# Kernel tuning notes

Measured on AMD Instinct MI355X. Metric: run time of the kernel, lower is better.

## Reference

```python
import jax, jax.numpy as jnp
import numpy as np

NUM_SKILLS = 1000
DIM_S = 64
SIZE_M = 64
B, T = 64, 200


def setup_inputs() -> dict:
    key = jax.random.key(0)
    ks = jax.random.split(key, 16)
    skills = jax.random.randint(ks[0], (B, T), 0, NUM_SKILLS)
    responses = jax.random.randint(ks[1], (B, T), 0, 2)
    s = 1.0 / np.sqrt(DIM_S)
    return {
        "skills": skills,
        "responses": responses,
        "k_emb": jax.random.normal(ks[2], (NUM_SKILLS, DIM_S)) * s,
        "v_emb": jax.random.normal(ks[3], (2 * NUM_SKILLS, DIM_S)) * s,
        "Mk": jax.random.normal(ks[4], (SIZE_M, DIM_S)) * np.sqrt(2.0 / DIM_S),
        "Mv0": jax.random.normal(ks[5], (SIZE_M, DIM_S)) * np.sqrt(2.0 / DIM_S),
        "fW": jax.random.normal(ks[6], (DIM_S, 2 * DIM_S)) * (1.0 / np.sqrt(2 * DIM_S)),
        "fb": jnp.zeros((DIM_S,)),
        "eW": jax.random.normal(ks[7], (DIM_S, DIM_S)) * s,
        "eb": jnp.zeros((DIM_S,)),
        "aW": jax.random.normal(ks[8], (DIM_S, DIM_S)) * s,
        "ab": jnp.zeros((DIM_S,)),
        "pW": jax.random.normal(ks[9], (1, DIM_S)) * s,
        "pb": jnp.zeros((1,)),
    }


def reference(skills, responses, k_emb, v_emb, Mk, Mv0, fW, fb, eW, eb, aW, ab, pW, pb):
    # dropout is identity in eval mode
    masked_r = responses * (responses > -1).astype(responses.dtype)
    x = skills + NUM_SKILLS * masked_r            # [B, T]
    k = k_emb[skills]                              # [B, T, D]
    v = v_emb[x]                                   # [B, T, D]
    w = jax.nn.softmax(jnp.einsum('btd,md->btm', k, Mk), axis=-1)  # [B, T, M]
    e = jax.nn.sigmoid(v @ eW.T + eb)              # [B, T, D]
    a = jnp.tanh(v @ aW.T + ab)                    # [B, T, D]

    Mv_init = jnp.broadcast_to(Mv0, (skills.shape[0],) + Mv0.shape)  # [B, M, D]

    def step(Mvt, inp):
        wt, et, at = inp                           # [B,M], [B,D], [B,D]
        read = jnp.einsum('bm,bmd->bd', wt, Mvt)   # read BEFORE update (Mv[:, :-1])
        Mvt = Mvt * (1.0 - wt[:, :, None] * et[:, None, :]) + wt[:, :, None] * at[:, None, :]
        return Mvt, read

    xs = (jnp.swapaxes(w, 0, 1), jnp.swapaxes(e, 0, 1), jnp.swapaxes(a, 0, 1))
    _, reads = jax.lax.scan(step, Mv_init, xs)     # reads: [T, B, D]
    reads = jnp.swapaxes(reads, 0, 1)              # [B, T, D]

    f = jnp.tanh(jnp.concatenate([reads, k], axis=-1) @ fW.T + fb)  # [B, T, D]
    p = jax.nn.sigmoid(f @ pW.T + pb)[..., 0]      # [B, T]
    return p[:, 1:]                                # pred, [B, T-1]
```

## Files before the change

kernel.cpp:

```cpp
#include <hip/hip_runtime.h>
#include <hip/hip_bf16.h>
#include <stdint.h>

#define NSK 1000
#define TT  200
#define BB  64
#define NROW (BB * TT)
#define NOUT (BB * (TT-1))
#define CH  20
#define RW  8

__device__ __forceinline__ float lane_bcast(float v, int l) {
  return __uint_as_float(__builtin_amdgcn_readlane(__float_as_uint(v), l));
}
__device__ __forceinline__ unsigned ulane_bcast(unsigned v, int l) {
  return __builtin_amdgcn_readlane(v, l);
}
__device__ __forceinline__ float frcp(float x) { return __builtin_amdgcn_rcpf(x); }
__device__ __forceinline__ float sigm(float x) { return frcp(1.f + __expf(-x)); }
__device__ __forceinline__ float tanh_fast(float x) {
  return fmaf(-2.f, frcp(1.f + __expf(2.f * x)), 1.f);
}

typedef _Float16 half2v __attribute__((ext_vector_type(2)));
union H2U { unsigned u; half2v h; };
__device__ __forceinline__ unsigned pack2h(float a, float b) {
  H2U x; x.h = (half2v){(_Float16)a, (_Float16)b}; return x.u;
}
__device__ __forceinline__ unsigned short f16bits(float x) {
  H2U u; u.h = (half2v){(_Float16)x, (_Float16)0.f}; return (unsigned short)(u.u & 0xffffu);
}
__device__ __forceinline__ float f16lo(unsigned bits) {
  H2U u; u.u = bits; return (float)u.h.x;
}
__device__ __forceinline__ float f16hi(unsigned bits) {
  H2U u; u.u = bits; return (float)u.h.y;
}
__device__ __forceinline__ float dot2h(unsigned sp, unsigned wp, float acc) {
#if __has_builtin(__builtin_amdgcn_fdot2)
  H2U s, w; s.u = sp; w.u = wp;
  return __builtin_amdgcn_fdot2(s.h, w.h, acc, false);
#else
  H2U s, w; s.u = sp; w.u = wp;
  return fmaf((float)s.h.y, (float)w.h.y, fmaf((float)s.h.x, (float)w.h.x, acc));
#endif
}
__device__ __forceinline__ unsigned pack_pairs(float v) {
  const int lane = threadIdx.x & 63;
  float a = __shfl(v, 2 * lane);
  float b = __shfl(v, 2 * lane + 1);
  return pack2h(a, b);
}

__global__ __launch_bounds__(256) void wea_kernel(
    const int* __restrict__ skills, const int* __restrict__ responses,
    const float* __restrict__ k_emb, const float* __restrict__ v_emb,
    const float* __restrict__ Mk, const float* __restrict__ eW,
    const float* __restrict__ eb, const float* __restrict__ aW,
    const float* __restrict__ ab,
    unsigned* __restrict__ ea_ws, unsigned short* __restrict__ w16_ws)
{
  __shared__ unsigned sw[3 * 64 * 40];
  const int tid = threadIdx.x;
  for (int ch = tid; ch < 1536; ch += 256) {
    const int mat = ch >> 9, rem = ch & 511;
    const int j = rem >> 3, cc = rem & 7;
    const float4* src = (mat == 0) ? (const float4*)Mk
                      : (mat == 1) ? (const float4*)eW : (const float4*)aW;
    const float4 f0 = src[j * 16 + cc * 2];
    const float4 f1 = src[j * 16 + cc * 2 + 1];
    uint4 pk;
    pk.x = pack2h(f0.x, f0.y); pk.y = pack2h(f0.z, f0.w);
    pk.z = pack2h(f1.x, f1.y); pk.w = pack2h(f1.z, f1.w);
    *(uint4*)&sw[mat * 2560 + j * 40 + ((cc + j) & 7) * 4] = pk;
  }
  __syncthreads();

  const int wave = tid >> 6, lane = tid & 63;
  const float ebl = eb[lane], abl = ab[lane];
  const int r0 = (blockIdx.x * 4 + wave) * 2;

  float kv[2], vv[2];
  #pragma unroll
  for (int i = 0; i < 2; ++i) {
    const int sk = skills[r0 + i];
    int rr = responses[r0 + i]; rr = (rr > -1) ? rr : 0;
    kv[i] = k_emb[(size_t)sk * 64 + lane];
    vv[i] = v_emb[(size_t)(sk + NSK * rr) * 64 + lane];
  }
  unsigned kp[2], vp[2];
  #pragma unroll
  for (int i = 0; i < 2; ++i) { kp[i] = pack_pairs(kv[i]); vp[i] = pack_pairs(vv[i]); }

  float accK[2] = {0.f, 0.f}, accE[2] = {0.f, 0.f}, accA[2] = {0.f, 0.f};
  #pragma unroll 1
  for (int h = 0; h < 2; ++h) {
    uint4 qm[4], qe[4], qa[4];
    #pragma unroll
    for (int c = 0; c < 4; ++c) {
      const int off = lane * 40 + (((h * 4 + c) + lane) & 7) * 4;
      qm[c] = *(const uint4*)&sw[off];
      qe[c] = *(const uint4*)&sw[2560 + off];
      qa[c] = *(const uint4*)&sw[5120 + off];
    }
    #pragma unroll
    for (int i = 0; i < 2; ++i) {
      #pragma unroll
      for (int c = 0; c < 4; ++c) {
        const unsigned um[4] = {qm[c].x, qm[c].y, qm[c].z, qm[c].w};
        const unsigned ue[4] = {qe[c].x, qe[c].y, qe[c].z, qe[c].w};
        const unsigned ua[4] = {qa[c].x, qa[c].y, qa[c].z, qa[c].w};
        #pragma unroll
        for (int m = 0; m < 4; ++m) {
          const int idx = (h * 4 + c) * 4 + m;
          const unsigned spk = ulane_bcast(kp[i], idx);
          const unsigned spv = ulane_bcast(vp[i], idx);
          accK[i] = dot2h(spk, um[m], accK[i]);
          accE[i] = dot2h(spv, ue[m], accE[i]);
          accA[i] = dot2h(spv, ua[m], accA[i]);
        }
      }
    }
  }
  #pragma unroll
  for (int i = 0; i < 2; ++i) {
    const int row = r0 + i;
    float mx = accK[i];
    #pragma unroll
    for (int off = 32; off; off >>= 1) mx = fmaxf(mx, __shfl_xor(mx, off));
    float ex = __expf(accK[i] - mx);
    float sm = ex;
    #pragma unroll
    for (int off = 32; off; off >>= 1) sm += __shfl_xor(sm, off);
    const float wv  = ex * frcp(sm);
    const float evv = sigm(accE[i] + ebl);
    const float avv = tanh_fast(accA[i] + abl);
    ea_ws[(size_t)row * 64 + lane]  = pack2h(evv, avv);
    w16_ws[(size_t)row * 64 + lane] = f16bits(wv);
  }
}

__device__ __forceinline__ void load_chunk(
    const unsigned* __restrict__ eap, const unsigned short* __restrict__ wp,
    int t0, int wl, int lane, unsigned* eab, unsigned* wvb)
{
  #pragma unroll
  for (int k = 0; k < CH; ++k) {
    eab[k] = eap[(t0 + k) * 64 + lane];
    wvb[k] = (unsigned)wp[(t0 + k) * 64 + wl];
  }
}

__device__ __forceinline__ void compute_chunk(
    float* Mv, const unsigned* eab, const unsigned* wvb,
    float* __restrict__ red, int wave, int lane)
{
  #pragma unroll
  for (int k = 0; k < CH; ++k) {
    const float ev = f16lo(eab[k]), av = f16hi(eab[k]);
    float rp = 0.f;
    #pragma unroll
    for (int i = 0; i < RW; ++i) {
      const float wm = f16lo(ulane_bcast(wvb[k], i));
      rp = fmaf(wm, Mv[i], rp);
      float tp = fmaf(-ev, Mv[i], av);
      Mv[i] = fmaf(wm, tp, Mv[i]);
    }
    red[k * 256 + wave * 64 + lane] = rp;
  }
}

__device__ __forceinline__ void reduce_store(
    const float* __restrict__ red, int ch, int base, int wave, int lane,
    unsigned short* __restrict__ ps)
{
  #pragma unroll
  for (int u = 0; u < 5; ++u) {
    const int k = wave * 5 + u;
    const float* rr = red + k * 256;
    const float v = (rr[lane] + rr[64 + lane]) + (rr[128 + lane] + rr[192 + lane]);
    ps[(size_t)(base + ch * CH + k) * 64 + lane] = f16bits(v);
  }
}

__global__ __launch_bounds__(256) void scan_kernel(
    const float* __restrict__ Mv0,
    const unsigned* __restrict__ ea_ws, const unsigned short* __restrict__ w16_ws,
    unsigned short* __restrict__ p0, unsigned short* __restrict__ p1)
{
  __shared__ float red[2][CH * 256];
  const int b    = blockIdx.x >> 1;
  const int s    = blockIdx.x & 1;
  const int wave = threadIdx.x >> 6;
  const int lane = threadIdx.x & 63;
  const int base = b * TT;
  const int m0   = s * 32 + wave * RW;
  const int wl   = m0 + (lane & (RW - 1));
  unsigned short* ps = s ? p1 : p0;

  float Mv[RW];
  #pragma unroll
  for (int i = 0; i < RW; ++i) Mv[i] = Mv0[(size_t)(m0 + i) * 64 + lane];

  const unsigned* eap = ea_ws + (size_t)base * 64;
  const unsigned short* wp = w16_ws + (size_t)base * 64;

  unsigned ea0[CH], wv0[CH], ea1[CH], wv1[CH];
  load_chunk(eap, wp, 0, wl, lane, ea0, wv0);
  for (int ch = 0; ch < TT / CH; ch += 2) {
    if ((ch + 1) * CH < TT)
      load_chunk(eap, wp, (ch + 1) * CH, wl, lane, ea1, wv1);
    compute_chunk(Mv, ea0, wv0, red[0], wave, lane);
    __syncthreads();
    reduce_store(red[0], ch, base, wave, lane, ps);
    if ((ch + 2) * CH < TT)
      load_chunk(eap, wp, (ch + 2) * CH, wl, lane, ea0, wv0);
    if ((ch + 1) * CH < TT) {
      compute_chunk(Mv, ea1, wv1, red[1], wave, lane);
      __syncthreads();
      reduce_store(red[1], ch + 1, base, wave, lane, ps);
    }
  }
}

__global__ __launch_bounds__(256) void fp_kernel(
    const int* __restrict__ skills, const float* __restrict__ k_emb,
    const float* __restrict__ fW, const float* __restrict__ fb,
    const float* __restrict__ pW, const float* __restrict__ pb,
    const unsigned short* __restrict__ p0, const unsigned short* __restrict__ p1,
    float* __restrict__ out)
{
  __shared__ unsigned sf[64 * 72];
  const int tid = threadIdx.x;
  for (int ch = tid; ch < 1024; ch += 256) {
    const int j = ch >> 4, cc = ch & 15;
    const float4 f0 = ((const float4*)fW)[j * 32 + cc * 2];
    const float4 f1 = ((const float4*)fW)[j * 32 + cc * 2 + 1];
    uint4 pk;
    pk.x = pack2h(f0.x, f0.y); pk.y = pack2h(f0.z, f0.w);
    pk.z = pack2h(f1.x, f1.y); pk.w = pack2h(f1.z, f1.w);
    *(uint4*)&sf[j * 72 + ((cc + j) & 15) * 4] = pk;
  }
  __syncthreads();

  const int wave = tid >> 6, lane = tid & 63;
  const float fbl = fb[lane], pwl = pW[lane], pb0 = pb[0];
  const int p = blockIdx.x * 4 + wave;

  float rv[2], kc[2];
  int bsave[2], tsave[2];
  #pragma unroll
  for (int i = 0; i < 2; ++i) {
    const unsigned idx = 2u * p + i;
    const unsigned b = idx / 199u;
    const int row = (int)(idx + b + 1u);
    bsave[i] = (int)b; tsave[i] = (int)(idx - b * 199u);
    rv[i] = f16lo((unsigned)p0[(size_t)row * 64 + lane])
          + f16lo((unsigned)p1[(size_t)row * 64 + lane]);
    kc[i] = k_emb[(size_t)skills[row] * 64 + lane];
  }
  unsigned rvp[2], kvp[2];
  #pragma unroll
  for (int i = 0; i < 2; ++i) {
    rvp[i] = pack_pairs(rv[i]);
    kvp[i] = pack_pairs(kc[i]);
  }

  float acc[2] = {fbl, fbl};
  #pragma unroll 1
  for (int h = 0; h < 4; ++h) {
    uint4 qf[4];
    #pragma unroll
    for (int c = 0; c < 4; ++c)
      qf[c] = *(const uint4*)&sf[lane * 72 + (((h * 4 + c) + lane) & 15) * 4];
    #pragma unroll
    for (int i = 0; i < 2; ++i) {
      #pragma unroll
      for (int c = 0; c < 4; ++c) {
        const unsigned uu[4] = {qf[c].x, qf[c].y, qf[c].z, qf[c].w};
        #pragma unroll
        for (int m = 0; m < 4; ++m) {
          const int idx = (h * 4 + c) * 4 + m;
          const unsigned sp = (idx < 32) ? ulane_bcast(rvp[i], idx)
                                         : ulane_bcast(kvp[i], idx - 32);
          acc[i] = dot2h(sp, uu[m], acc[i]);
        }
      }
    }
  }

  float f0 = tanh_fast(acc[0]) * pwl;
  float f1 = tanh_fast(acc[1]) * pwl;
  #pragma unroll
  for (int off = 32; off; off >>= 1) {
    f0 += __shfl_xor(f0, off);
    f1 += __shfl_xor(f1, off);
  }
  if (lane == 0) {
    out[(size_t)bsave[0] * (TT - 1) + tsave[0]] = sigm(f0 + pb0);
    out[(size_t)bsave[1] * (TT - 1) + tsave[1]] = sigm(f1 + pb0);
  }
}

extern "C" void kernel_launch(void* const* d_in, const int* in_sizes, int n_in,
                              void* d_out, int out_size, void* d_ws, size_t ws_size,
                              hipStream_t stream) {
  const int* skills    = (const int*)d_in[0];
  const int* responses = (const int*)d_in[1];
  const float* k_emb   = (const float*)d_in[2];
  const float* v_emb   = (const float*)d_in[3];
  const float* Mk      = (const float*)d_in[4];
  const float* Mv0     = (const float*)d_in[5];
  const float* fW      = (const float*)d_in[6];
  const float* fb      = (const float*)d_in[7];
  const float* eW      = (const float*)d_in[8];
  const float* eb      = (const float*)d_in[9];
  const float* aW      = (const float*)d_in[10];
  const float* ab      = (const float*)d_in[11];
  const float* pW      = (const float*)d_in[12];
  const float* pb      = (const float*)d_in[13];

  unsigned* ea_ws       = (unsigned*)d_ws;
  unsigned short* w16_ws = (unsigned short*)(ea_ws + (size_t)NROW * 64);
  unsigned short* p0    = w16_ws + (size_t)NROW * 64;
  unsigned short* p1    = p0 + (size_t)NROW * 64;

  wea_kernel<<<dim3(NROW / 8), 256, 0, stream>>>(
      skills, responses, k_emb, v_emb, Mk, eW, eb, aW, ab, ea_ws, w16_ws);
  scan_kernel<<<dim3(BB * 2), 256, 0, stream>>>(Mv0, ea_ws, w16_ws, p0, p1);
  fp_kernel<<<dim3(NOUT / 8), 256, 0, stream>>>(
      skills, k_emb, fW, fb, pW, pb, p0, p1, (float*)d_out);
}
```

Before: 128.7 us.

## Store packed fp16 partial reads and keys; process four rows per wave in fp_kernel

The scan kernel now writes its partial reads as packed half2 pairs with 32 lanes storing, instead of one fp16 per lane. wea_kernel also writes a packed fp16 copy of each row's key embedding, so fp_kernel no longer gathers skills and k_emb or repacks them. fp_kernel sums the two partials with a packed half add and handles four rows per wave over half as many blocks, amortising the fW staging in shared memory. Costs are an extra workspace write in wea_kernel, partial sums added in fp16 rather than fp32, and fewer blocks in fp_kernel.

```diff
diff --git a/kernel.cpp b/kernel.cpp
--- a/kernel.cpp
+++ b/kernel.cpp
@@ -35,6 +35,9 @@
 }
 __device__ __forceinline__ float f16hi(unsigned bits) {
   H2U u; u.u = bits; return (float)u.h.y;
+}
+__device__ __forceinline__ unsigned pkadd(unsigned a, unsigned b) {
+  H2U x, y, r; x.u = a; y.u = b; r.h = x.h + y.h; return r.u;
 }
 __device__ __forceinline__ float dot2h(unsigned sp, unsigned wp, float acc) {
 #if __has_builtin(__builtin_amdgcn_fdot2)
@@ -58,7 +61,8 @@
     const float* __restrict__ Mk, const float* __restrict__ eW,
     const float* __restrict__ eb, const float* __restrict__ aW,
     const float* __restrict__ ab,
-    unsigned* __restrict__ ea_ws, unsigned short* __restrict__ w16_ws)
+    unsigned* __restrict__ ea_ws, unsigned short* __restrict__ w16_ws,
+    unsigned* __restrict__ k16p_ws)
 {
   __shared__ unsigned sw[3 * 64 * 40];
   const int tid = threadIdx.x;
@@ -91,6 +95,9 @@
   unsigned kp[2], vp[2];
   #pragma unroll
   for (int i = 0; i < 2; ++i) { kp[i] = pack_pairs(kv[i]); vp[i] = pack_pairs(vv[i]); }
+  #pragma unroll
+  for (int i = 0; i < 2; ++i)
+    if (lane < 32) k16p_ws[(size_t)(r0 + i) * 32 + lane] = kp[i];
 
   float accK[2] = {0.f, 0.f}, accE[2] = {0.f, 0.f}, accA[2] = {0.f, 0.f};
   #pragma unroll 1
@@ -172,21 +179,22 @@
 
 __device__ __forceinline__ void reduce_store(
     const float* __restrict__ red, int ch, int base, int wave, int lane,
-    unsigned short* __restrict__ ps)
+    unsigned* __restrict__ ps)
 {
   #pragma unroll
   for (int u = 0; u < 5; ++u) {
     const int k = wave * 5 + u;
     const float* rr = red + k * 256;
     const float v = (rr[lane] + rr[64 + lane]) + (rr[128 + lane] + rr[192 + lane]);
-    ps[(size_t)(base + ch * CH + k) * 64 + lane] = f16bits(v);
+    const unsigned pv = pack_pairs(v);
+    if (lane < 32) ps[(size_t)(base + ch * CH + k) * 32 + lane] = pv;
   }
 }
 
 __global__ __launch_bounds__(256) void scan_kernel(
     const float* __restrict__ Mv0,
     const unsigned* __restrict__ ea_ws, const unsigned short* __restrict__ w16_ws,
-    unsigned short* __restrict__ p0, unsigned short* __restrict__ p1)
+    unsigned* __restrict__ p0, unsigned* __restrict__ p1)
 {
   __shared__ float red[2][CH * 256];
   const int b    = blockIdx.x >> 1;
@@ -196,7 +204,7 @@
   const int base = b * TT;
   const int m0   = s * 32 + wave * RW;
   const int wl   = m0 + (lane & (RW - 1));
-  unsigned short* ps = s ? p1 : p0;
+  unsigned* ps = s ? p1 : p0;
 
   float Mv[RW];
   #pragma unroll
@@ -224,11 +232,10 @@
 }
 
 __global__ __launch_bounds__(256) void fp_kernel(
-    const int* __restrict__ skills, const float* __restrict__ k_emb,
     const float* __restrict__ fW, const float* __restrict__ fb,
     const float* __restrict__ pW, const float* __restrict__ pb,
-    const unsigned short* __restrict__ p0, const unsigned short* __restrict__ p1,
-    float* __restrict__ out)
+    const unsigned* __restrict__ p0, const unsigned* __restrict__ p1,
+    const unsigned* __restrict__ k16p, float* __restrict__ out)
 {
   __shared__ unsigned sf[64 * 72];
   const int tid = threadIdx.x;
@@ -243,30 +250,23 @@
   }
   __syncthreads();
 
-  const int wave = tid >> 6, lane = tid & 63;
+  const int wave = tid >> 6, lane = tid & 63, l31 = lane & 31;
   const float fbl = fb[lane], pwl = pW[lane], pb0 = pb[0];
-  const int p = blockIdx.x * 4 + wave;
-
-  float rv[2], kc[2];
-  int bsave[2], tsave[2];
-  #pragma unroll
-  for (int i = 0; i < 2; ++i) {
-    const unsigned idx = 2u * p + i;
-    const unsigned b = idx / 199u;
-    const int row = (int)(idx + b + 1u);
-    bsave[i] = (int)b; tsave[i] = (int)(idx - b * 199u);
-    rv[i] = f16lo((unsigned)p0[(size_t)row * 64 + lane])
-          + f16lo((unsigned)p1[(size_t)row * 64 + lane]);
-    kc[i] = k_emb[(size_t)skills[row] * 64 + lane];
-  }
-  unsigned rvp[2], kvp[2];
-  #pragma unroll
-  for (int i = 0; i < 2; ++i) {
-    rvp[i] = pack_pairs(rv[i]);
-    kvp[i] = pack_pairs(kc[i]);
-  }
-
-  float acc[2] = {fbl, fbl};
+  const int g = blockIdx.x * 4 + wave;
+
+  unsigned rvp[4], kvp[4];
+  int bsave[4], tsave[4];
+  #pragma unroll
+  for (int i = 0; i < 4; ++i) {
+    const unsigned idx = 4u * g + i;
+    const unsigned bb_ = idx / 199u;
+    const int row = (int)(idx + bb_ + 1u);
+    bsave[i] = (int)bb_; tsave[i] = (int)(idx - bb_ * 199u);
+    rvp[i] = pkadd(p0[(size_t)row * 32 + l31], p1[(size_t)row * 32 + l31]);
+    kvp[i] = k16p[(size_t)row * 32 + l31];
+  }
+
+  float acc[4] = {fbl, fbl, fbl, fbl};
   #pragma unroll 1
   for (int h = 0; h < 4; ++h) {
     uint4 qf[4];
@@ -274,7 +274,7 @@
     for (int c = 0; c < 4; ++c)
       qf[c] = *(const uint4*)&sf[lane * 72 + (((h * 4 + c) + lane) & 15) * 4];
     #pragma unroll
-    for (int i = 0; i < 2; ++i) {
+    for (int i = 0; i < 4; ++i) {
       #pragma unroll
       for (int c = 0; c < 4; ++c) {
         const unsigned uu[4] = {qf[c].x, qf[c].y, qf[c].z, qf[c].w};
@@ -289,16 +289,13 @@
     }
   }
 
-  float f0 = tanh_fast(acc[0]) * pwl;
-  float f1 = tanh_fast(acc[1]) * pwl;
-  #pragma unroll
-  for (int off = 32; off; off >>= 1) {
-    f0 += __shfl_xor(f0, off);
-    f1 += __shfl_xor(f1, off);
-  }
-  if (lane == 0) {
-    out[(size_t)bsave[0] * (TT - 1) + tsave[0]] = sigm(f0 + pb0);
-    out[(size_t)bsave[1] * (TT - 1) + tsave[1]] = sigm(f1 + pb0);
+  #pragma unroll
+  for (int i = 0; i < 4; ++i) {
+    float f = tanh_fast(acc[i]) * pwl;
+    #pragma unroll
+    for (int off = 32; off; off >>= 1) f += __shfl_xor(f, off);
+    if (lane == 0)
+      out[(size_t)bsave[i] * (TT - 1) + tsave[i]] = sigm(f + pb0);
   }
 }
 
@@ -320,14 +317,15 @@
   const float* pW      = (const float*)d_in[12];
   const float* pb      = (const float*)d_in[13];
 
-  unsigned* ea_ws       = (unsigned*)d_ws;
+  unsigned* ea_ws        = (unsigned*)d_ws;
   unsigned short* w16_ws = (unsigned short*)(ea_ws + (size_t)NROW * 64);
-  unsigned short* p0    = w16_ws + (size_t)NROW * 64;
-  unsigned short* p1    = p0 + (size_t)NROW * 64;
+  unsigned* p0           = (unsigned*)(w16_ws + (size_t)NROW * 64);
+  unsigned* p1           = p0 + (size_t)NROW * 32;
+  unsigned* k16p         = p1 + (size_t)NROW * 32;
 
   wea_kernel<<<dim3(NROW / 8), 256, 0, stream>>>(
-      skills, responses, k_emb, v_emb, Mk, eW, eb, aW, ab, ea_ws, w16_ws);
+      skills, responses, k_emb, v_emb, Mk, eW, eb, aW, ab, ea_ws, w16_ws, k16p);
   scan_kernel<<<dim3(BB * 2), 256, 0, stream>>>(Mv0, ea_ws, w16_ws, p0, p1);
-  fp_kernel<<<dim3(NOUT / 8), 256, 0, stream>>>(
-      skills, k_emb, fW, fb, pW, pb, p0, p1, (float*)d_out);
-}
+  fp_kernel<<<dim3(NOUT / 16), 256, 0, stream>>>(
+      fW, fb, pW, pb, p0, p1, k16p, (float*)d_out);
+}
```

Result: slower. 137.0 us (+6.5%).
